# Optimization experiments

Hardware: AMD Instinct MI355X
Metric: run time of the kernel (lower is better)

## Reference

```python
import jax, jax.numpy as jnp
import numpy as np

B, T, C, H = 4, 4096, 2048, 128


def setup_inputs() -> dict:
    key = jax.random.key(0)
    ks = jax.random.split(key, 7)
    s = 0.02
    return {
        "x": jax.random.normal(ks[0], (B, T, C), dtype=jnp.float32),
        "Wk": jax.random.normal(ks[1], (C, H), dtype=jnp.float32) * s,
        "bk": jax.random.normal(ks[2], (H,), dtype=jnp.float32) * s,
        "Wq": jax.random.normal(ks[3], (C, H), dtype=jnp.float32) * s,
        "bq": jax.random.normal(ks[4], (H,), dtype=jnp.float32) * s,
        "Wv": jax.random.normal(ks[5], (C, H), dtype=jnp.float32) * s,
        "bv": jax.random.normal(ks[6], (H,), dtype=jnp.float32) * s,
    }


def reference(x, Wk, bk, Wq, bq, Wv, bv):
    # x: [B, T, C]
    Bq, Tq, Cq = x.shape
    k = x @ Wk + bk  # [B, T, H]
    q = x @ Wq + bq
    v = x @ Wv + bv
    # NOTE: original scales by C**-0.5 (input emb dim), faithfully reproduced.
    scale = jnp.asarray(Cq, x.dtype) ** -0.5
    wei = jnp.einsum("bth,bsh->bts", q, k) * scale  # [B, T, T]
    causal = jnp.tril(jnp.ones((Tq, Tq), dtype=bool))
    wei = jnp.where(causal, wei, -jnp.inf)
    wei = jax.nn.softmax(wei, axis=-1)
    # dropout omitted (inference/eval mode)
    return jnp.einsum("bts,bsh->bth", wei, v)  # [B, T, H]
```

## Files before the change

### kernel.cpp

```cpp
#include <hip/hip_runtime.h>
#include <hip/hip_bf16.h>
#include <stdint.h>

#define T_SEQ 4096
#define C_DIM 2048
#define H_DIM 128
#define NBATCH 4

typedef unsigned short u16;
typedef __attribute__((ext_vector_type(8))) __bf16 bf16x8;
typedef __attribute__((ext_vector_type(4))) float f32x4;
typedef __attribute__((ext_vector_type(8))) unsigned short u16x8;
typedef __attribute__((ext_vector_type(4))) unsigned short u16x4;

__device__ __forceinline__ u16 f2bf(float f) {
  union { float f; uint32_t i; } v; v.f = f;
  uint32_t r = v.i + 0x7FFFu + ((v.i >> 16) & 1u);
  return (u16)(r >> 16);
}
__device__ __forceinline__ float bf2f(u16 u) {
  union { uint32_t i; float f; } v; v.i = ((uint32_t)u) << 16;
  return v.f;
}

__device__ __forceinline__ void gload16(const void* g, void* l) {
  __builtin_amdgcn_global_load_lds(
      (__attribute__((address_space(1))) void*)(g),
      (__attribute__((address_space(3))) void*)(l), 16, 0, 0);
}

__device__ __forceinline__ f32x4 mfma_bf16(bf16x8 a, bf16x8 b, f32x4 c) {
  return __builtin_amdgcn_mfma_f32_16x16x32_bf16(a, b, c, 0, 0, 0);
}

template<int CTRL>
__device__ __forceinline__ float dpp_mov(float x) {
  return __int_as_float(__builtin_amdgcn_mov_dpp(__float_as_int(x), CTRL, 0xF, 0xF, true));
}
__device__ __forceinline__ float red16_max(float v) {
  v = fmaxf(v, dpp_mov<0x121>(v));
  v = fmaxf(v, dpp_mov<0x122>(v));
  v = fmaxf(v, dpp_mov<0x124>(v));
  v = fmaxf(v, dpp_mov<0x128>(v));
  return v;
}
__device__ __forceinline__ float red16_sum(float v) {
  v += dpp_mov<0x121>(v);
  v += dpp_mov<0x122>(v);
  v += dpp_mov<0x124>(v);
  v += dpp_mov<0x128>(v);
  return v;
}

__global__ __launch_bounds__(256) void transpose_w(
    const float* __restrict__ Wq, const float* __restrict__ Wk,
    const float* __restrict__ Wv, u16* __restrict__ Wt)
{
  __shared__ u16 Wl[64 * 72];
  const int bk = blockIdx.x;
  const int bn = blockIdx.y;
  const int p  = blockIdx.z;
  const float* W = (p == 0) ? Wq : (p == 1) ? Wk : Wv;
  const int t = threadIdx.x;

  for (int ps = 0; ps < 16; ++ps) {
    int e  = ps * 256 + t;
    int kk = e >> 6, nn = e & 63;
    Wl[kk * 72 + nn] = f2bf(W[(size_t)(bk * 64 + kk) * H_DIM + bn * 64 + nn]);
  }
  __syncthreads();
  for (int ps = 0; ps < 16; ++ps) {
    int o  = ps * 256 + t;
    int nl = o >> 6, kl = o & 63;
    int n  = bn * 64 + nl;
    int g  = kl >> 3, j = kl & 7;
    int ks = ((g ^ (n & 7)) << 3) | j;
    Wt[(size_t)p * (H_DIM * C_DIM) + (size_t)n * C_DIM + bk * 64 + kl] = Wl[ks * 72 + nl];
  }
}

__global__ __launch_bounds__(512, 1) void qkv_fused(
    const float* __restrict__ x, const u16* __restrict__ Wt,
    const float* __restrict__ bq, const float* __restrict__ bk, const float* __restrict__ bv,
    u16* __restrict__ qo, u16* __restrict__ ko, u16* __restrict__ vTo)
{
  __shared__ alignas(16) u16 SMEM[2][28672];

  const int tid  = threadIdx.x;
  const int w    = tid >> 6, lane = tid & 63;
  const int t16  = lane & 15, quad = lane >> 4;
  const int mh   = w >> 2;
  const int nq   = w & 3;
  const int rt   = blockIdx.x;

  f32x4 acc[2][6];
  for (int i = 0; i < 2; ++i)
    for (int j = 0; j < 6; ++j) acc[i][j] = f32x4{0.f, 0.f, 0.f, 0.f};

  const size_t rowBase = (size_t)rt * 64;
  const int arow = tid >> 3;
  const int ag   = tid & 7;
  const float* xrow = &x[(rowBase + arow) * C_DIM + ag * 8];

  float4 a0 = ((const float4*)(xrow))[0];
  float4 a1 = ((const float4*)(xrow))[1];
  {
    u16* As = SMEM[0];
    u16* Bs = SMEM[0] + 4096;
    for (int p = 0; p < 3; ++p) {
      const u16* Wp = Wt + (size_t)p * (H_DIM * C_DIM);
      for (int j = 0; j < 2; ++j) {
        int e8 = (((j << 3) + w) * 64 + lane) * 8;
        int rr = e8 >> 6, kk = e8 & 63;
        gload16(Wp + (size_t)rr * C_DIM + kk, &Bs[p * 8192 + e8]);
      }
    }
    u16x8 pk;
    pk[0] = f2bf(a0.x); pk[1] = f2bf(a0.y); pk[2] = f2bf(a0.z); pk[3] = f2bf(a0.w);
    pk[4] = f2bf(a1.x); pk[5] = f2bf(a1.y); pk[6] = f2bf(a1.z); pk[7] = f2bf(a1.w);
    *(u16x8*)&As[arow * 64 + ((ag ^ (arow & 7)) << 3)] = pk;
  }
  a0 = ((const float4*)(xrow + 64))[0];
  a1 = ((const float4*)(xrow + 64))[1];

  for (int it = 0; it < 32; ++it) {
    const int cur = it & 1, nxt = cur ^ 1;
    __syncthreads();

    if (it + 1 < 32) {
      const int k1 = (it + 1) * 64;
      u16* As = SMEM[nxt];
      u16* Bs = SMEM[nxt] + 4096;
      for (int p = 0; p < 3; ++p) {
        const u16* Wp = Wt + (size_t)p * (H_DIM * C_DIM);
        for (int j = 0; j < 2; ++j) {
          int e8 = (((j << 3) + w) * 64 + lane) * 8;
          int rr = e8 >> 6, kk = e8 & 63;
          gload16(Wp + (size_t)rr * C_DIM + k1 + kk, &Bs[p * 8192 + e8]);
        }
      }
      u16x8 pk;
      pk[0] = f2bf(a0.x); pk[1] = f2bf(a0.y); pk[2] = f2bf(a0.z); pk[3] = f2bf(a0.w);
      pk[4] = f2bf(a1.x); pk[5] = f2bf(a1.y); pk[6] = f2bf(a1.z); pk[7] = f2bf(a1.w);
      *(u16x8*)&As[arow * 64 + ((ag ^ (arow & 7)) << 3)] = pk;
      if (it + 2 < 32) {
        const float4* xp = (const float4*)(xrow + (it + 2) * 64);
        a0 = xp[0]; a1 = xp[1];
      }
    }

    u16* As = SMEM[cur];
    u16* Bs = SMEM[cur] + 4096;
    for (int ks = 0; ks < 2; ++ks) {
      bf16x8 af[2], bfr[6];
      for (int ra = 0; ra < 2; ++ra)
        af[ra] = *(const bf16x8*)&As[(mh * 32 + ra * 16 + t16) * 64 +
                                     (((ks * 4 + quad) ^ (t16 & 7)) << 3)];
      for (int c = 0; c < 6; ++c) {
        int col = nq * 96 + c * 16 + t16;
        int p = col >> 7, pc = col & 127;
        bfr[c] = *(const bf16x8*)&Bs[p * 8192 + pc * 64 +
                                     (((ks * 4 + quad) ^ (t16 & 7)) << 3)];
      }
      for (int ra = 0; ra < 2; ++ra)
        for (int c = 0; c < 6; ++c)
          acc[ra][c] = mfma_bf16(af[ra], bfr[c], acc[ra][c]);
    }
  }

  __syncthreads();
  u16* Oq = SMEM[0];
  u16* Ok = SMEM[0] + 8192;
  u16* Ov = SMEM[0] + 16384;

  const float QSCALE = 0.022097086912079612f;
  for (int c = 0; c < 6; ++c) {
    int col = nq * 96 + c * 16 + t16;
    int p = col >> 7, pc = col & 127;
    float bias = (p == 0) ? bq[pc] : (p == 1) ? bk[pc] : bv[pc];
    for (int ra = 0; ra < 2; ++ra) {
      for (int r = 0; r < 4; ++r) {
        int row16 = mh * 32 + ra * 16 + quad * 4 + r;
        float v = acc[ra][c][r] + bias;
        if (p == 0) v *= QSCALE;
        if (p == 2) {
          int gt = row16 >> 3;
          Ov[pc * 64 + ((gt ^ (pc & 7)) << 3) + (row16 & 7)] = f2bf(v);
        } else {
          u16* O = (p == 0) ? Oq : Ok;
          int g = pc >> 3;
          O[row16 * 128 + (((g ^ (row16 & 15)) << 3) | (pc & 7))] = f2bf(v);
        }
      }
    }
  }
  __syncthreads();

  const int bb = rt >> 6;
  const int tb = (rt & 63) * 64;
  for (int ps = 0; ps < 2; ++ps) {
    int c = ps * 512 + tid;
    {
      int row16 = c >> 4, g = c & 15;
      u16x8 v = *(const u16x8*)&Oq[row16 * 128 + ((g ^ (row16 & 15)) << 3)];
      *(u16x8*)&qo[(rowBase + row16) * H_DIM + g * 8] = v;
    }
    *(u16x8*)&ko[rowBase * H_DIM + c * 8] = *(const u16x8*)&Ok[c * 8];
    {
      int d = c >> 3, gc = c & 7;
      *(u16x8*)&vTo[((size_t)bb * H_DIM + d) * T_SEQ + tb + gc * 8] =
          *(const u16x8*)&Ov[c * 8];
    }
  }
}

__global__ __launch_bounds__(256, 3) void flash_attn(
    const u16* __restrict__ q, const u16* __restrict__ k,
    const u16* __restrict__ vT, float* __restrict__ out,
    void* __restrict__ OpartRaw, float* __restrict__ MLpart,
    int split, int pf32)
{
  __shared__ alignas(16) u16 Kt[2][64 * 128];
  __shared__ alignas(16) u16 Ps[4 * 16 * 72];

  const int tid  = threadIdx.x;
  const int w    = tid >> 6, lane = tid & 63;
  const int t16  = lane & 15, quad = lane >> 4;
  const int b    = blockIdx.x;

  int qt, kt0, ktn, mls, esd;
  if (split) {
    const int j = blockIdx.y;
    int c, n;
    if (j < 64)       { qt = 63 - (j >> 2); c = j & 3; n = 4; }
    else if (j < 112) { int t = j - 64; int d3 = t / 3; qt = 47 - d3; c = t - d3 * 3; n = 3; }
    else if (j < 144) { int t = j - 112; qt = 31 - (t >> 1); c = t & 1; n = 2; }
    else              { qt = 159 - j; c = 0; n = 1; }
    const int NT = qt + 1;
    kt0 = c * NT / n;
    ktn = (c + 1) * NT / n - kt0;
    if (n == 1) { mls = -1; esd = -1; }
    else {
      int mlb, esb;
      if (qt >= 48)      { mlb = (qt - 48) * 4;       esb = (qt - 48) * 3; }
      else if (qt >= 32) { mlb = 64 + (qt - 32) * 3;  esb = 48 + (qt - 32) * 2; }
      else               { mlb = 112 + (qt - 16) * 2; esb = 80 + (qt - 16); }
      mls = b * 144 + mlb + c;
      esd = (c >= 1) ? (b * 96 + esb + c - 1) : -2;
    }
  } else {
    qt = 63 - blockIdx.y; kt0 = 0; ktn = qt + 1; mls = -1; esd = -1;
  }

  const float L2E = 1.4426950408889634f;

  bf16x8 qf[4];
  {
    const u16* qrow = q + ((size_t)(b * T_SEQ + qt * 64 + w * 16 + t16)) * H_DIM;
    for (int c = 0; c < 4; ++c)
      qf[c] = *(const bf16x8*)(qrow + c * 32 + quad * 8);
  }

  f32x4 Oc[8];
  for (int i = 0; i < 8; ++i) Oc[i] = f32x4{0.f, 0.f, 0.f, 0.f};
  float mrow[4] = {-1e30f, -1e30f, -1e30f, -1e30f};
  float lrow[4] = {0.f, 0.f, 0.f, 0.f};

  const u16* kbase = k  + ((size_t)b * T_SEQ) * H_DIM;
  const u16* vbase = vT + ((size_t)b * H_DIM) * T_SEQ;

  {
    const u16* kg = kbase + (size_t)(kt0 * 64) * H_DIM;
    for (int j = 0; j < 4; ++j) {
      int e8 = (((j << 2) + w) * 64 + lane) * 8;
      gload16(kg + e8, &Kt[0][e8]);
    }
  }

  int cur = 0;
  for (int it = 0; it < ktn; ++it) {
    const int kt = kt0 + it;
    __syncthreads();
    if (it + 1 < ktn) {
      const int nb = cur ^ 1;
      const u16* kg = kbase + (size_t)((kt + 1) * 64) * H_DIM;
      for (int j = 0; j < 4; ++j) {
        int e8 = (((j << 2) + w) * 64 + lane) * 8;
        gload16(kg + e8, &Kt[nb][e8]);
      }
    }

    f32x4 S[4];
    for (int ct = 0; ct < 4; ++ct) S[ct] = f32x4{0.f, 0.f, 0.f, 0.f};
    __builtin_amdgcn_s_setprio(1);
    for (int c = 0; c < 4; ++c) {
      for (int ct = 0; ct < 4; ++ct) {
        bf16x8 kf = *(const bf16x8*)&Kt[cur][(ct * 16 + t16) * H_DIM +
                                            (((c * 4 + quad) ^ t16) << 3)];
        S[ct] = mfma_bf16(qf[c], kf, S[ct]);
      }
    }
    __builtin_amdgcn_s_setprio(0);

    const u16* vg = vbase + kt * 64;
    bf16x8 vf[2][8];
    for (int ks = 0; ks < 2; ++ks)
      for (int dt = 0; dt < 8; ++dt)
        vf[ks][dt] = *(const bf16x8*)&vg[(size_t)(dt * 16 + t16) * T_SEQ +
                                         (((ks * 4 + quad) ^ (t16 & 7)) << 3)];

    if (kt == qt) {
      for (int ct = 0; ct < 4; ++ct)
        for (int r = 0; r < 4; ++r)
          if (ct * 16 + t16 > w * 16 + quad * 4 + r) S[ct][r] = -1e30f;
    }

    float alpha[4];
    bool any = false;
    for (int r = 0; r < 4; ++r) {
      float mx = red16_max(fmaxf(fmaxf(S[0][r], S[1][r]), fmaxf(S[2][r], S[3][r])));
      if (mx > mrow[r] + 8.0f) {
        alpha[r] = exp2f((mrow[r] - mx) * L2E);
        mrow[r] = mx;
        any = true;
      } else {
        alpha[r] = 1.0f;
      }
    }
    if (any) {
      for (int r = 0; r < 4; ++r) lrow[r] *= alpha[r];
      for (int dt = 0; dt < 8; ++dt)
        for (int r = 0; r < 4; ++r)
          Oc[dt][r] *= alpha[r];
    }
    for (int r = 0; r < 4; ++r) {
      float s = 0.f;
      for (int ct = 0; ct < 4; ++ct) {
        float pv = exp2f((S[ct][r] - mrow[r]) * L2E);
        S[ct][r] = pv;
        s += pv;
      }
      lrow[r] += red16_sum(s);
    }

    u16* pw = &Ps[w * 1152];
    for (int ct = 0; ct < 4; ++ct)
      for (int r = 0; r < 4; ++r)
        pw[(quad * 4 + r) * 72 + ct * 16 + t16] = f2bf(S[ct][r]);
    __asm__ volatile("s_waitcnt lgkmcnt(0)" ::: "memory");

    __builtin_amdgcn_s_setprio(1);
    for (int ks = 0; ks < 2; ++ks) {
      bf16x8 pf = *(const bf16x8*)&pw[t16 * 72 + ks * 32 + quad * 8];
      for (int dt = 0; dt < 8; ++dt)
        Oc[dt] = mfma_bf16(pf, vf[ks][dt], Oc[dt]);
    }
    __builtin_amdgcn_s_setprio(0);
    cur ^= 1;
  }

  if (mls < 0) {
    for (int r = 0; r < 4; ++r) {
      float inv = 1.0f / lrow[r];
      size_t row = (size_t)b * T_SEQ + qt * 64 + w * 16 + quad * 4 + r;
      for (int dt = 0; dt < 8; ++dt)
        out[row * H_DIM + dt * 16 + t16] = Oc[dt][r] * inv;
    }
  } else {
    if (t16 == 0)
      for (int r = 0; r < 4; ++r) {
        int row = w * 16 + quad * 4 + r;
        MLpart[(size_t)mls * 128 + row * 2 + 0] = mrow[r];
        MLpart[(size_t)mls * 128 + row * 2 + 1] = lrow[r];
      }
    if (esd == -2) {
      for (int r = 0; r < 4; ++r) {
        size_t row = (size_t)b * T_SEQ + qt * 64 + w * 16 + quad * 4 + r;
        for (int dt = 0; dt < 8; ++dt)
          out[row * H_DIM + dt * 16 + t16] = Oc[dt][r];
      }
    } else if (pf32) {
      float* op = (float*)OpartRaw + (size_t)esd * 8192;
      for (int r = 0; r < 4; ++r) {
        int row = w * 16 + quad * 4 + r;
        for (int dt = 0; dt < 8; ++dt)
          op[row * 128 + dt * 16 + t16] = Oc[dt][r];
      }
    } else {
      u16* op = (u16*)OpartRaw + (size_t)esd * 8192;
      for (int r = 0; r < 4; ++r) {
        int row = w * 16 + quad * 4 + r;
        for (int dt = 0; dt < 8; ++dt)
          op[row * 128 + dt * 16 + t16] = f2bf(Oc[dt][r]);
      }
    }
  }
}

__global__ __launch_bounds__(256) void combine(
    const void* __restrict__ OpartRaw, const float* __restrict__ MLpart,
    float* __restrict__ out, int pf32)
{
  __shared__ float cs[4][64];
  const float L2E = 1.4426950408889634f;
  const int s = blockIdx.x;
  const int b = s / 48, qt = 16 + (s % 48);
  const int t = threadIdx.x;

  int n, mlb, esb;
  if (qt >= 48)      { n = 4; mlb = (qt - 48) * 4;       esb = (qt - 48) * 3; }
  else if (qt >= 32) { n = 3; mlb = 64 + (qt - 32) * 3;  esb = 48 + (qt - 32) * 2; }
  else               { n = 2; mlb = 112 + (qt - 16) * 2; esb = 80 + (qt - 16); }
  const int mls0 = b * 144 + mlb;
  const int esd0 = b * 96 + esb;

  if (t < 64) {
    float m[4], l[4];
    float mg = -1e30f;
    for (int c = 0; c < n; ++c) {
      const float* ML = MLpart + (size_t)(mls0 + c) * 128;
      m[c] = ML[t * 2]; l[c] = ML[t * 2 + 1];
      mg = fmaxf(mg, m[c]);
    }
    float denom = 0.f, e[4];
    for (int c = 0; c < n; ++c) {
      e[c] = exp2f((m[c] - mg) * L2E);
      denom += l[c] * e[c];
    }
    float inv = 1.0f / denom;
    for (int c = 0; c < n; ++c) cs[c][t] = e[c] * inv;
  }
  __syncthreads();

  float* o = out + ((size_t)b * T_SEQ + (size_t)qt * 64) * (size_t)H_DIM;
  for (int i4 = t; i4 < 2048; i4 += 256) {
    const int row = i4 >> 5;
    float4 acc = ((float4*)o)[i4];
    const float c0 = cs[0][row];
    acc.x *= c0; acc.y *= c0; acc.z *= c0; acc.w *= c0;
    for (int c = 1; c < n; ++c) {
      const float cc = cs[c][row];
      if (pf32) {
        const float4 p = ((const float4*)((const float*)OpartRaw +
                          (size_t)(esd0 + c - 1) * 8192))[i4];
        acc.x += p.x * cc; acc.y += p.y * cc;
        acc.z += p.z * cc; acc.w += p.w * cc;
      } else {
        const u16x4 p = ((const u16x4*)((const u16*)OpartRaw +
                         (size_t)(esd0 + c - 1) * 8192))[i4];
        acc.x += bf2f(p[0]) * cc; acc.y += bf2f(p[1]) * cc;
        acc.z += bf2f(p[2]) * cc; acc.w += bf2f(p[3]) * cc;
      }
    }
    ((float4*)o)[i4] = acc;
  }
}

extern "C" void kernel_launch(void* const* d_in, const int* in_sizes, int n_in,
                              void* d_out, int out_size, void* d_ws, size_t ws_size,
                              hipStream_t stream) {
  const float* x  = (const float*)d_in[0];
  const float* Wk = (const float*)d_in[1];
  const float* bk = (const float*)d_in[2];
  const float* Wq = (const float*)d_in[3];
  const float* bq = (const float*)d_in[4];
  const float* Wv = (const float*)d_in[5];
  const float* bv = (const float*)d_in[6];
  float* out = (float*)d_out;

  char* ws = (char*)d_ws;
  u16* qb  = (u16*)(ws);
  u16* kb  = (u16*)(ws + 4194304);
  u16* vT  = (u16*)(ws + 8388608);
  u16* Wt  = (u16*)(ws + 12582912);
  void* Opart = (void*)(ws + 14155776);

  const size_t base     = 14155776ull;
  const size_t ml_bytes = 294912ull;
  const size_t need_f32 = base + 12582912ull + ml_bytes;
  const size_t need_b16 = base + 6291456ull  + ml_bytes;

  int split, pf32;
  float* MLpart;
  if (ws_size >= need_f32) {
    split = 1; pf32 = 1;
    MLpart = (float*)(ws + base + 12582912ull);
  } else if (ws_size >= need_b16) {
    split = 1; pf32 = 0;
    MLpart = (float*)(ws + base + 6291456ull);
  } else {
    split = 0; pf32 = 0;
    MLpart = (float*)(ws + base);
  }

  hipLaunchKernelGGL(transpose_w, dim3(32, 2, 3), dim3(256), 0, stream, Wq, Wk, Wv, Wt);
  hipLaunchKernelGGL(qkv_fused, dim3(256), dim3(512), 0, stream,
                     x, Wt, bq, bk, bv, qb, kb, vT);
  hipLaunchKernelGGL(flash_attn, dim3(4, split ? 160 : 64), dim3(256), 0, stream,
                     qb, kb, vT, out, Opart, MLpart, split, pf32);
  if (split)
    hipLaunchKernelGGL(combine, dim3(192), dim3(256), 0, stream, Opart, MLpart, out, pf32);
}
```

Measured before the change: 297.6 us.

## Split QKV projection grid across Q/K/V outputs for more blocks and occupancy

The QKV projection kernel now launches one block per (row tile, projection) with 256 threads instead of one 512-thread block computing all three projections. Each block holds a smaller shared-memory footprint and accumulator set, so up to three blocks can share a CU and the grid grows from 256 to 768 blocks on a 256-CU class GPU. In exchange, each 64-row tile of x is read from global memory and converted to bf16 three times instead of once.

```diff
diff --git a/kernel.cpp b/kernel.cpp
--- a/kernel.cpp
+++ b/kernel.cpp
@@ -79,49 +79,59 @@
   }
 }
 
-__global__ __launch_bounds__(512, 1) void qkv_fused(
+__global__ __launch_bounds__(256, 3) void qkv_fused(
     const float* __restrict__ x, const u16* __restrict__ Wt,
     const float* __restrict__ bq, const float* __restrict__ bk, const float* __restrict__ bv,
     u16* __restrict__ qo, u16* __restrict__ ko, u16* __restrict__ vTo)
 {
-  __shared__ alignas(16) u16 SMEM[2][28672];
+  __shared__ alignas(16) u16 SMEM[2][12288];
 
   const int tid  = threadIdx.x;
   const int w    = tid >> 6, lane = tid & 63;
   const int t16  = lane & 15, quad = lane >> 4;
-  const int mh   = w >> 2;
-  const int nq   = w & 3;
+  const int mh   = w >> 1;
+  const int nq   = w & 1;
   const int rt   = blockIdx.x;
-
-  f32x4 acc[2][6];
+  const int p    = blockIdx.y;
+
+  const u16* Wp = Wt + (size_t)p * (H_DIM * C_DIM);
+  const float* bias_p = (p == 0) ? bq : (p == 1) ? bk : bv;
+
+  f32x4 acc[2][4];
   for (int i = 0; i < 2; ++i)
-    for (int j = 0; j < 6; ++j) acc[i][j] = f32x4{0.f, 0.f, 0.f, 0.f};
+    for (int j = 0; j < 4; ++j) acc[i][j] = f32x4{0.f, 0.f, 0.f, 0.f};
 
   const size_t rowBase = (size_t)rt * 64;
   const int arow = tid >> 3;
   const int ag   = tid & 7;
-  const float* xrow = &x[(rowBase + arow) * C_DIM + ag * 8];
-
-  float4 a0 = ((const float4*)(xrow))[0];
-  float4 a1 = ((const float4*)(xrow))[1];
+  const float* xr0 = &x[(rowBase + arow) * C_DIM + ag * 8];
+  const float* xr1 = &x[(rowBase + arow + 32) * C_DIM + ag * 8];
+  const int aswz = ((ag ^ (arow & 7)) << 3);
+
+  float4 a0 = ((const float4*)xr0)[0];
+  float4 a1 = ((const float4*)xr0)[1];
+  float4 a2 = ((const float4*)xr1)[0];
+  float4 a3 = ((const float4*)xr1)[1];
   {
     u16* As = SMEM[0];
     u16* Bs = SMEM[0] + 4096;
-    for (int p = 0; p < 3; ++p) {
-      const u16* Wp = Wt + (size_t)p * (H_DIM * C_DIM);
-      for (int j = 0; j < 2; ++j) {
-        int e8 = (((j << 3) + w) * 64 + lane) * 8;
-        int rr = e8 >> 6, kk = e8 & 63;
-        gload16(Wp + (size_t)rr * C_DIM + kk, &Bs[p * 8192 + e8]);
-      }
+    for (int j = 0; j < 4; ++j) {
+      int e8 = (j * 256 + tid) * 8;
+      int rr = e8 >> 6, kk = e8 & 63;
+      gload16(Wp + (size_t)rr * C_DIM + kk, &Bs[e8]);
     }
     u16x8 pk;
     pk[0] = f2bf(a0.x); pk[1] = f2bf(a0.y); pk[2] = f2bf(a0.z); pk[3] = f2bf(a0.w);
     pk[4] = f2bf(a1.x); pk[5] = f2bf(a1.y); pk[6] = f2bf(a1.z); pk[7] = f2bf(a1.w);
-    *(u16x8*)&As[arow * 64 + ((ag ^ (arow & 7)) << 3)] = pk;
-  }
-  a0 = ((const float4*)(xrow + 64))[0];
-  a1 = ((const float4*)(xrow + 64))[1];
+    *(u16x8*)&As[arow * 64 + aswz] = pk;
+    pk[0] = f2bf(a2.x); pk[1] = f2bf(a2.y); pk[2] = f2bf(a2.z); pk[3] = f2bf(a2.w);
+    pk[4] = f2bf(a3.x); pk[5] = f2bf(a3.y); pk[6] = f2bf(a3.z); pk[7] = f2bf(a3.w);
+    *(u16x8*)&As[(arow + 32) * 64 + aswz] = pk;
+  }
+  a0 = ((const float4*)(xr0 + 64))[0];
+  a1 = ((const float4*)(xr0 + 64))[1];
+  a2 = ((const float4*)(xr1 + 64))[0];
+  a3 = ((const float4*)(xr1 + 64))[1];
 
   for (int it = 0; it < 32; ++it) {
     const int cur = it & 1, nxt = cur ^ 1;
@@ -131,53 +141,49 @@
       const int k1 = (it + 1) * 64;
       u16* As = SMEM[nxt];
       u16* Bs = SMEM[nxt] + 4096;
-      for (int p = 0; p < 3; ++p) {
-        const u16* Wp = Wt + (size_t)p * (H_DIM * C_DIM);
-        for (int j = 0; j < 2; ++j) {
-          int e8 = (((j << 3) + w) * 64 + lane) * 8;
-          int rr = e8 >> 6, kk = e8 & 63;
-          gload16(Wp + (size_t)rr * C_DIM + k1 + kk, &Bs[p * 8192 + e8]);
-        }
+      for (int j = 0; j < 4; ++j) {
+        int e8 = (j * 256 + tid) * 8;
+        int rr = e8 >> 6, kk = e8 & 63;
+        gload16(Wp + (size_t)rr * C_DIM + k1 + kk, &Bs[e8]);
       }
       u16x8 pk;
       pk[0] = f2bf(a0.x); pk[1] = f2bf(a0.y); pk[2] = f2bf(a0.z); pk[3] = f2bf(a0.w);
       pk[4] = f2bf(a1.x); pk[5] = f2bf(a1.y); pk[6] = f2bf(a1.z); pk[7] = f2bf(a1.w);
-      *(u16x8*)&As[arow * 64 + ((ag ^ (arow & 7)) << 3)] = pk;
+      *(u16x8*)&As[arow * 64 + aswz] = pk;
+      pk[0] = f2bf(a2.x); pk[1] = f2bf(a2.y); pk[2] = f2bf(a2.z); pk[3] = f2bf(a2.w);
+      pk[4] = f2bf(a3.x); pk[5] = f2bf(a3.y); pk[6] = f2bf(a3.z); pk[7] = f2bf(a3.w);
+      *(u16x8*)&As[(arow + 32) * 64 + aswz] = pk;
       if (it + 2 < 32) {
-        const float4* xp = (const float4*)(xrow + (it + 2) * 64);
-        a0 = xp[0]; a1 = xp[1];
+        const float4* xp0 = (const float4*)(xr0 + (it + 2) * 64);
+        const float4* xp1 = (const float4*)(xr1 + (it + 2) * 64);
+        a0 = xp0[0]; a1 = xp0[1]; a2 = xp1[0]; a3 = xp1[1];
       }
     }
 
     u16* As = SMEM[cur];
     u16* Bs = SMEM[cur] + 4096;
     for (int ks = 0; ks < 2; ++ks) {
-      bf16x8 af[2], bfr[6];
+      bf16x8 af[2], bfr[4];
+      const int ksz = (((ks * 4 + quad) ^ (t16 & 7)) << 3);
       for (int ra = 0; ra < 2; ++ra)
-        af[ra] = *(const bf16x8*)&As[(mh * 32 + ra * 16 + t16) * 64 +
-                                     (((ks * 4 + quad) ^ (t16 & 7)) << 3)];
-      for (int c = 0; c < 6; ++c) {
-        int col = nq * 96 + c * 16 + t16;
-        int p = col >> 7, pc = col & 127;
-        bfr[c] = *(const bf16x8*)&Bs[p * 8192 + pc * 64 +
-                                     (((ks * 4 + quad) ^ (t16 & 7)) << 3)];
+        af[ra] = *(const bf16x8*)&As[(mh * 32 + ra * 16 + t16) * 64 + ksz];
+      for (int c = 0; c < 4; ++c) {
+        int col = nq * 64 + c * 16 + t16;
+        bfr[c] = *(const bf16x8*)&Bs[col * 64 + ksz];
       }
       for (int ra = 0; ra < 2; ++ra)
-        for (int c = 0; c < 6; ++c)
+        for (int c = 0; c < 4; ++c)
           acc[ra][c] = mfma_bf16(af[ra], bfr[c], acc[ra][c]);
     }
   }
 
   __syncthreads();
-  u16* Oq = SMEM[0];
-  u16* Ok = SMEM[0] + 8192;
-  u16* Ov = SMEM[0] + 16384;
+  u16* O = SMEM[0];
 
   const float QSCALE = 0.022097086912079612f;
-  for (int c = 0; c < 6; ++c) {
-    int col = nq * 96 + c * 16 + t16;
-    int p = col >> 7, pc = col & 127;
-    float bias = (p == 0) ? bq[pc] : (p == 1) ? bk[pc] : bv[pc];
+  for (int c = 0; c < 4; ++c) {
+    int pc = nq * 64 + c * 16 + t16;
+    float bias = bias_p[pc];
     for (int ra = 0; ra < 2; ++ra) {
       for (int r = 0; r < 4; ++r) {
         int row16 = mh * 32 + ra * 16 + quad * 4 + r;
@@ -185,9 +191,8 @@
         if (p == 0) v *= QSCALE;
         if (p == 2) {
           int gt = row16 >> 3;
-          Ov[pc * 64 + ((gt ^ (pc & 7)) << 3) + (row16 & 7)] = f2bf(v);
+          O[pc * 64 + ((gt ^ (pc & 7)) << 3) + (row16 & 7)] = f2bf(v);
         } else {
-          u16* O = (p == 0) ? Oq : Ok;
           int g = pc >> 3;
           O[row16 * 128 + (((g ^ (row16 & 15)) << 3) | (pc & 7))] = f2bf(v);
         }
@@ -198,18 +203,18 @@
 
   const int bb = rt >> 6;
   const int tb = (rt & 63) * 64;
-  for (int ps = 0; ps < 2; ++ps) {
-    int c = ps * 512 + tid;
-    {
+  for (int j = 0; j < 4; ++j) {
+    int c = j * 256 + tid;
+    if (p == 0) {
       int row16 = c >> 4, g = c & 15;
-      u16x8 v = *(const u16x8*)&Oq[row16 * 128 + ((g ^ (row16 & 15)) << 3)];
+      u16x8 v = *(const u16x8*)&O[row16 * 128 + ((g ^ (row16 & 15)) << 3)];
       *(u16x8*)&qo[(rowBase + row16) * H_DIM + g * 8] = v;
-    }
-    *(u16x8*)&ko[rowBase * H_DIM + c * 8] = *(const u16x8*)&Ok[c * 8];
-    {
+    } else if (p == 1) {
+      *(u16x8*)&ko[rowBase * H_DIM + c * 8] = *(const u16x8*)&O[c * 8];
+    } else {
       int d = c >> 3, gc = c & 7;
       *(u16x8*)&vTo[((size_t)bb * H_DIM + d) * T_SEQ + tb + gc * 8] =
-          *(const u16x8*)&Ov[c * 8];
+          *(const u16x8*)&O[c * 8];
     }
   }
 }
@@ -494,7 +499,7 @@
   }
 
   hipLaunchKernelGGL(transpose_w, dim3(32, 2, 3), dim3(256), 0, stream, Wq, Wk, Wv, Wt);
-  hipLaunchKernelGGL(qkv_fused, dim3(256), dim3(512), 0, stream,
+  hipLaunchKernelGGL(qkv_fused, dim3(256, 3), dim3(256), 0, stream,
                      x, Wt, bq, bk, bv, qb, kb, vT);
   hipLaunchKernelGGL(flash_attn, dim3(4, split ? 160 : 64), dim3(256), 0, stream,
                      qb, kb, vT, out, Opart, MLpart, split, pf32);
```

Result: no change. 299.4 us (+0.6%).
